# Kernel tuning notes

Hardware: AMD Instinct MI355X
Metric: run time of the kernel (lower is better)

Reference implementation:

```python
import jax, jax.numpy as jnp
import numpy as np

B, L, SD, PD, H, HD, OH = 2, 256, 64, 32, 4, 16, 32
EXP = 64  # MBConv hidden = pair_dim * expand_ratio(2)
SE = 16   # squeezed channels = int(64 * 0.25)


def _ln(x, g, b, eps=1e-5):
    m = jnp.mean(x, -1, keepdims=True)
    v = jnp.mean((x - m) ** 2, -1, keepdims=True)
    return (x - m) / jnp.sqrt(v + eps) * g + b


def _inorm(x, eps=1e-5):  # InstanceNorm2d (no affine), x: [B,C,H,W]
    m = jnp.mean(x, (2, 3), keepdims=True)
    v = jnp.mean((x - m) ** 2, (2, 3), keepdims=True)
    return (x - m) / jnp.sqrt(v + eps)


def setup_inputs() -> dict:
    key = jax.random.key(0)
    ks = jax.random.split(key, 16)
    s = jnp.float32(0.02)
    return dict(
        seq_repr=jax.random.normal(ks[0], (B, L, SD), jnp.float32),
        pair_repr=jax.random.normal(ks[1], (B, L, L, PD), jnp.float32),
        g_attn=jnp.ones((SD,), jnp.float32), b_attn=jnp.zeros((SD,), jnp.float32),
        g_pair=jnp.ones((PD,), jnp.float32), b_pair=jnp.zeros((PD,), jnp.float32),
        W_opm_lin=jax.random.normal(ks[2], (SD, OH), jnp.float32) * s,
        b_opm_lin=jnp.zeros((OH,), jnp.float32),
        g_opm=jnp.ones((OH * OH,), jnp.float32), b_opm=jnp.zeros((OH * OH,), jnp.float32),
        W_opm_proj=jax.random.normal(ks[3], (OH * OH, PD), jnp.float32) * s,
        b_opm_proj=jnp.zeros((PD,), jnp.float32),
        W_exp=jax.random.normal(ks[4], (EXP, PD), jnp.float32) * s,
        W_dw=jax.random.normal(ks[5], (EXP, 1, 3, 3), jnp.float32) * s,
        W_se1=jax.random.normal(ks[6], (SE, EXP), jnp.float32) * s,
        b_se1=jnp.zeros((SE,), jnp.float32),
        W_se2=jax.random.normal(ks[7], (EXP, SE), jnp.float32) * s,
        b_se2=jnp.zeros((EXP,), jnp.float32),
        W_pw=jax.random.normal(ks[8], (PD, EXP), jnp.float32) * s,
        W_qkv=jax.random.normal(ks[9], (SD, 3 * SD), jnp.float32) * s,
        W_outp=jax.random.normal(ks[10], (SD, SD), jnp.float32) * s,
        b_outp=jnp.zeros((SD,), jnp.float32),
        W_bias=jax.random.normal(ks[11], (PD, H), jnp.float32) * s,
    )


def reference(seq_repr, pair_repr, g_attn, b_attn, g_pair, b_pair,
              W_opm_lin, b_opm_lin, g_opm, b_opm, W_opm_proj, b_opm_proj,
              W_exp, W_dw, W_se1, b_se1, W_se2, b_se2, W_pw,
              W_qkv, W_outp, b_outp, W_bias):
    # --- OuterProductMean on attn_norm(seq) ---
    x = _ln(seq_repr, g_attn, b_attn)                            # [B,L,SD]
    a = x @ W_opm_lin + b_opm_lin                                # [B,L,OH]
    outer = jnp.einsum('bid,bje->bijde', a, a).reshape(B, L, L, OH * OH)
    op = _ln(outer, g_opm, b_opm) @ W_opm_proj + b_opm_proj      # [B,L,L,PD]
    pair = pair_repr + op
    # --- MBConv pair processor on pair_norm(pair) ---
    pn = _ln(pair, g_pair, b_pair)
    z0 = jnp.transpose(pn, (0, 3, 1, 2))                         # NCHW [B,PD,L,L]
    h = jax.nn.silu(_inorm(jnp.einsum('bcij,oc->boij', z0, W_exp)))
    h = jax.lax.conv_general_dilated(h, W_dw, (1, 1), 'SAME',
                                     feature_group_count=EXP,
                                     dimension_numbers=('NCHW', 'OIHW', 'NCHW'))
    h = jax.nn.silu(_inorm(h))
    sq = jnp.mean(h, (2, 3), keepdims=True)                      # squeeze [B,EXP,1,1]
    sq = jax.nn.silu(jnp.einsum('bcij,oc->boij', sq, W_se1) + b_se1[None, :, None, None])
    sq = jax.nn.sigmoid(jnp.einsum('bcij,oc->boij', sq, W_se2) + b_se2[None, :, None, None])
    h = h * sq
    h = _inorm(jnp.einsum('bcij,oc->boij', h, W_pw))             # project back to PD
    pair = pair + jnp.transpose(z0 + h, (0, 2, 3, 1))            # MBConv residual + outer residual
    # --- Pairwise-bias attention ---
    pn2 = _ln(pair, g_pair, b_pair)
    bias = jnp.einsum('bijp,ph->bhij', pn2, W_bias)              # [B,H,L,L]
    q, k, v = jnp.split(x @ W_qkv, 3, axis=-1)
    q = q.reshape(B, L, H, HD).transpose(0, 2, 1, 3)
    k = k.reshape(B, L, H, HD).transpose(0, 2, 1, 3)
    v = v.reshape(B, L, H, HD).transpose(0, 2, 1, 3)
    scores = jnp.einsum('bhid,bhjd->bhij', q, k) / jnp.sqrt(jnp.float32(HD)) + bias
    w = jax.nn.softmax(scores, axis=-1)
    ctx = jnp.einsum('bhij,bhjd->bhid', w, v).transpose(0, 2, 1, 3).reshape(B, L, SD)
    seq = seq_repr + ctx @ W_outp + b_outp
    return seq, pair
```

## Files before the change

### kernel.cpp

```cpp
#include <hip/hip_runtime.h>
#include <hip/hip_bf16.h>

#define LLSZ 65536
#define INV_LL (1.f / 65536.f)


__device__ __forceinline__ void chan_stats(const float* sum, const float* sumsq,
                                           int chan, float& m, float& isd)
{
    m = sum[chan] * INV_LL;
    float var = sumsq[chan] * INV_LL - m * m;
    isd = rsqrtf(var + 1e-5f);
}

__device__ __forceinline__ float silu(float t) { return t / (1.f + expf(-t)); }

__global__ __launch_bounds__(256) void kA(
    const float* __restrict__ g_opm, const float* __restrict__ b_opm,
    const float* __restrict__ Wproj, const float* __restrict__ b_proj,
    float* __restrict__ G, float* __restrict__ GW, float* __restrict__ BW,
    float* __restrict__ stats0,
    const float* __restrict__ seq, const float* __restrict__ g_attn,
    const float* __restrict__ b_attn, const float* __restrict__ W_lin,
    const float* __restrict__ b_lin, const float* __restrict__ W_qkv,
    float* __restrict__ a, float* __restrict__ am, float* __restrict__ s2,
    float* __restrict__ qkv)
{
    int tid = threadIdx.x;
    if (blockIdx.x == 0) {
        for (int k = tid; k < 768; k += 256) stats0[k] = 0.f;
        int p = tid & 31, rg = tid >> 5;
        float gw = 0.f, bw = 0.f;
        #pragma unroll 8
        for (int k = 0; k < 128; ++k) {
            int de = k * 8 + rg;
            float wv = Wproj[de * 32 + p];
            float gv = g_opm[de] * wv;
            G[de * 32 + p] = gv;
            gw += gv;
            bw += b_opm[de] * wv;
        }
        __shared__ float rG[256], rB[256];
        rG[rg * 32 + p] = gw;
        rB[rg * 32 + p] = bw;
        __syncthreads();
        for (int s = 4; s > 0; s >>= 1) {
            if (rg < s) {
                rG[rg * 32 + p] += rG[(rg + s) * 32 + p];
                rB[rg * 32 + p] += rB[(rg + s) * 32 + p];
            }
            __syncthreads();
        }
        if (tid < 32) { GW[p] = rG[p]; BW[p] = rB[p] + b_proj[p]; }
    } else {
        __shared__ float Wq[64 * 192];
        __shared__ float Wl[64 * 32];
        __shared__ float xL[4][64];
        #pragma unroll
        for (int k = 0; k < 48; ++k) Wq[k * 256 + tid] = W_qkv[k * 256 + tid];
        #pragma unroll
        for (int k = 0; k < 8; ++k) Wl[k * 256 + tid] = W_lin[k * 256 + tid];
        int sub = tid >> 6, t = tid & 63;
        int row = (blockIdx.x - 1) * 4 + sub;
        float v = seq[row * 64 + t];
        float m = v;
        for (int k = 32; k > 0; k >>= 1) m += __shfl_xor(m, k, 64);
        m *= (1.f / 64.f);
        float d = v - m;
        float var = d * d;
        for (int k = 32; k > 0; k >>= 1) var += __shfl_xor(var, k, 64);
        var *= (1.f / 64.f);
        float x = d * rsqrtf(var + 1e-5f) * g_attn[t] + b_attn[t];
        xL[sub][t] = x;
        __syncthreads();
        if (t < 32) {
            float s = 0.f;
            #pragma unroll
            for (int dd = 0; dd < 64; ++dd) s += xL[sub][dd] * Wl[dd * 32 + t];
            s += b_lin[t];
            a[row * 32 + t] = s;
            float mm = s, ss = s * s;
            for (int k = 16; k > 0; k >>= 1) {
                mm += __shfl_xor(mm, k, 32);
                ss += __shfl_xor(ss, k, 32);
            }
            if (t == 0) { am[row] = mm * (1.f / 32.f); s2[row] = ss * (1.f / 32.f); }
        }
        #pragma unroll
        for (int c3 = 0; c3 < 3; ++c3) {
            int c = c3 * 64 + t;
            float s = 0.f;
            #pragma unroll
            for (int dd = 0; dd < 64; ++dd) s += xL[sub][dd] * Wq[dd * 192 + c];
            qkv[row * 192 + c] = s;
        }
    }
}

__global__ __launch_bounds__(256) void k2_T(
    const float* __restrict__ a, const float* __restrict__ G, float* __restrict__ T)
{
    int row = blockIdx.x;
    int tid = threadIdx.x;
    __shared__ float aL[32];
    if (tid < 32) aL[tid] = a[row * 32 + tid];
    __syncthreads();
    for (int k = 0; k < 4; ++k) {
        int idx = k * 256 + tid;
        float s = 0.f;
        #pragma unroll
        for (int d = 0; d < 32; ++d) s += aL[d] * G[d * 1024 + idx];
        T[row * 1024 + idx] = s;
    }
}

__global__ __launch_bounds__(256) void k3_op(
    const float* __restrict__ a, const float* __restrict__ am,
    const float* __restrict__ s2, const float* __restrict__ T,
    const float* __restrict__ GW, const float* __restrict__ BW,
    const float* __restrict__ pair_in, float* __restrict__ pair1)
{
    int blk = blockIdx.x;
    int row = blk >> 3;
    int jg = blk & 7;
    int b = row >> 8;
    int j0 = jg * 32;
    int tid = threadIdx.x;
    __shared__ float Tl[1024];
    __shared__ float aL[32 * 33];
    __shared__ float amL[32], s2L[32], gwL[32], bwL[32];
    ((float4*)Tl)[tid] = ((const float4*)(T + (long)row * 1024))[tid];
    for (int k = 0; k < 4; ++k) {
        int idx = k * 256 + tid;
        aL[(idx >> 5) * 33 + (idx & 31)] = a[(b * 256 + j0) * 32 + idx];
    }
    if (tid < 32) {
        amL[tid] = am[b * 256 + j0 + tid];
        s2L[tid] = s2[b * 256 + j0 + tid];
        gwL[tid] = GW[tid];
        bwL[tid] = BW[tid];
    }
    __syncthreads();
    int jl = tid >> 3, cq = tid & 7;
    float am_i = am[row], s2_i = s2[row];
    float m = am_i * amL[jl];
    float isd = rsqrtf(s2_i * s2L[jl] - m * m + 1e-5f);
    long base = ((long)row * 256 + j0 + jl) * 32 + cq * 4;
    float4 pv = *(const float4*)(pair_in + base);
    float o[4];
    #pragma unroll
    for (int u = 0; u < 4; ++u) {
        int p = cq * 4 + u;
        float S = 0.f;
        #pragma unroll
        for (int e = 0; e < 32; ++e) S += aL[jl * 33 + e] * Tl[e * 32 + p];
        o[u] = isd * (S - m * gwL[p]) + bwL[p];
    }
    pv.x += o[0]; pv.y += o[1]; pv.z += o[2]; pv.w += o[3];
    *(float4*)(pair1 + base) = pv;
}

__global__ __launch_bounds__(256) void k4_expand(
    const float* __restrict__ pair1, const float* __restrict__ g_pair,
    const float* __restrict__ b_pair, const float* __restrict__ W_exp,
    float* __restrict__ e1, float* __restrict__ st1s, float* __restrict__ st1q)
{
    int blk = blockIdx.x;
    int b = blk >> 10;
    int pixbase = (blk & 1023) * 64;
    int tid = threadIdx.x;
    __shared__ float xL[64 * 33];
    __shared__ float We[2048];
    __shared__ float muL[64], isdL[64];
    __shared__ float gL[32], bL[32];
    for (int k = 0; k < 8; ++k) We[k * 256 + tid] = W_exp[k * 256 + tid];
    if (tid < 32) { gL[tid] = g_pair[tid]; bL[tid] = b_pair[tid]; }
    const float4* src = (const float4*)(pair1 + ((long)b * LLSZ + pixbase) * 32);
    #pragma unroll
    for (int k = 0; k < 2; ++k) {
        int idx = k * 256 + tid;
        float4 v = src[idx];
        int pix = idx >> 3, cq = idx & 7;
        xL[pix * 33 + cq * 4 + 0] = v.x;
        xL[pix * 33 + cq * 4 + 1] = v.y;
        xL[pix * 33 + cq * 4 + 2] = v.z;
        xL[pix * 33 + cq * 4 + 3] = v.w;
    }
    __syncthreads();
    if (tid < 64) {
        float s = 0.f, q = 0.f;
        #pragma unroll
        for (int c = 0; c < 32; ++c) { float v = xL[tid * 33 + c]; s += v; q += v * v; }
        float mu = s * (1.f / 32.f);
        muL[tid] = mu;
        isdL[tid] = rsqrtf(q * (1.f / 32.f) - mu * mu + 1e-5f);
    }
    __syncthreads();
    #pragma unroll
    for (int k = 0; k < 8; ++k) {
        int idx = k * 256 + tid;
        int pix = idx >> 5, c = idx & 31;
        xL[pix * 33 + c] = (xL[pix * 33 + c] - muL[pix]) * isdL[pix] * gL[c] + bL[c];
    }
    __syncthreads();
    int pix = tid & 63, og = tid >> 6;
    float ssk = 0.f, qqk = 0.f;
    for (int oo = 0; oo < 16; ++oo) {
        int o = og * 16 + oo;
        float acc = 0.f;
        #pragma unroll
        for (int c = 0; c < 32; ++c) acc += xL[pix * 33 + c] * We[o * 32 + c];
        e1[((long)(b * 64 + o)) * LLSZ + pixbase + pix] = acc;
        float s = acc, q = acc * acc;
        for (int k = 32; k > 0; k >>= 1) { s += __shfl_xor(s, k, 64); q += __shfl_xor(q, k, 64); }
        if (pix == oo) { ssk = s; qqk = q; }
    }
    if (pix < 16) {
        atomicAdd(&st1s[b * 64 + og * 16 + pix], ssk);
        atomicAdd(&st1q[b * 64 + og * 16 + pix], qqk);
    }
}

__global__ __launch_bounds__(256) void k6_dw(
    const float* __restrict__ e1, const float* __restrict__ st1s,
    const float* __restrict__ st1q, const float* __restrict__ W_dw,
    float* __restrict__ h2, float* __restrict__ st2s, float* __restrict__ st2q)
{
    int blk = blockIdx.x;
    int chan = blk >> 5;
    int r0 = (blk & 31) * 8;
    int o = chan & 63;
    int tid = threadIdx.x;
    float m, isd;
    chan_stats(st1s, st1q, chan, m, isd);
    __shared__ float sL[10][258];
    const float* src = e1 + (long)chan * LLSZ;
    for (int k = tid; k < 640; k += 256) {
        int rr = k >> 6, c4 = k & 63;
        int g = r0 - 1 + rr;
        float4 v = make_float4(0.f, 0.f, 0.f, 0.f);
        bool ok = (g >= 0 && g < 256);
        if (ok) v = *(const float4*)(src + g * 256 + c4 * 4);
        float t;
        t = (v.x - m) * isd; v.x = ok ? silu(t) : 0.f;
        t = (v.y - m) * isd; v.y = ok ? silu(t) : 0.f;
        t = (v.z - m) * isd; v.z = ok ? silu(t) : 0.f;
        t = (v.w - m) * isd; v.w = ok ? silu(t) : 0.f;
        sL[rr][1 + c4 * 4 + 0] = v.x;
        sL[rr][1 + c4 * 4 + 1] = v.y;
        sL[rr][1 + c4 * 4 + 2] = v.z;
        sL[rr][1 + c4 * 4 + 3] = v.w;
    }
    if (tid < 10) { sL[tid][0] = 0.f; sL[tid][257] = 0.f; }
    float w[9];
    #pragma unroll
    for (int k = 0; k < 9; ++k) w[k] = W_dw[o * 9 + k];
    __syncthreads();
    int c = tid;
    float bs = 0.f, bq = 0.f;
    #pragma unroll
    for (int rr = 0; rr < 8; ++rr) {
        float s = 0.f;
        #pragma unroll
        for (int ki = 0; ki < 3; ++ki)
            #pragma unroll
            for (int kj = 0; kj < 3; ++kj)
                s += sL[rr + ki][c + kj] * w[ki * 3 + kj];
        h2[(long)chan * LLSZ + (r0 + rr) * 256 + c] = s;
        bs += s; bq += s * s;
    }
    for (int k = 32; k > 0; k >>= 1) { bs += __shfl_xor(bs, k, 64); bq += __shfl_xor(bq, k, 64); }
    __shared__ float r2s[4], r2q[4];
    int wave = tid >> 6;
    if ((tid & 63) == 0) { r2s[wave] = bs; r2q[wave] = bq; }
    __syncthreads();
    if (tid == 0) {
        atomicAdd(&st2s[chan], r2s[0] + r2s[1] + r2s[2] + r2s[3]);
        atomicAdd(&st2q[chan], r2q[0] + r2q[1] + r2q[2] + r2q[3]);
    }
}

__global__ __launch_bounds__(256) void k8_squeeze(
    const float* __restrict__ h2, const float* __restrict__ st2s,
    const float* __restrict__ st2q, float* __restrict__ sqs)
{
    int bid = blockIdx.x;
    int chan = bid >> 3, seg = bid & 7;
    int tid = threadIdx.x;
    float m, isd;
    chan_stats(st2s, st2q, chan, m, isd);
    const float4* p = (const float4*)(h2 + (long)chan * LLSZ + seg * 8192);
    float s = 0.f;
    #pragma unroll
    for (int k = 0; k < 8; ++k) {
        float4 v = p[k * 256 + tid];
        s += silu((v.x - m) * isd) + silu((v.y - m) * isd)
           + silu((v.z - m) * isd) + silu((v.w - m) * isd);
    }
    for (int k = 32; k > 0; k >>= 1) s += __shfl_xor(s, k, 64);
    __shared__ float rs[4];
    int wave = tid >> 6;
    if ((tid & 63) == 0) rs[wave] = s;
    __syncthreads();
    if (tid == 0) atomicAdd(&sqs[chan], rs[0] + rs[1] + rs[2] + rs[3]);
}

__global__ __launch_bounds__(256) void k10_pw(
    const float* __restrict__ h2, const float* __restrict__ st2s,
    const float* __restrict__ st2q, const float* __restrict__ sqs,
    const float* __restrict__ W_se1, const float* __restrict__ b_se1,
    const float* __restrict__ W_se2, const float* __restrict__ b_se2,
    const float* __restrict__ W_pw, float* __restrict__ hp,
    float* __restrict__ st3s, float* __restrict__ st3q)
{
    int blk = blockIdx.x;
    int b = blk >> 10;
    int pixbase = (blk & 1023) * 64;
    int tid = threadIdx.x;
    __shared__ float hL[64 * 65];
    __shared__ float Wp[2048];
    __shared__ float s1L[16];
    __shared__ float sqvL[64];
    for (int k = 0; k < 8; ++k) Wp[k * 256 + tid] = W_pw[k * 256 + tid];
    if (tid < 16) {
        float s = 0.f;
        for (int c = 0; c < 64; ++c) s += sqs[b * 64 + c] * W_se1[tid * 64 + c];
        s = s * INV_LL + b_se1[tid];
        s1L[tid] = silu(s);
    }
    __syncthreads();
    if (tid < 64) {
        float s = 0.f;
        #pragma unroll
        for (int j = 0; j < 16; ++j) s += s1L[j] * W_se2[tid * 16 + j];
        s += b_se2[tid];
        sqvL[tid] = 1.f / (1.f + expf(-s));
    }
    __syncthreads();
    #pragma unroll
    for (int k = 0; k < 4; ++k) {
        int idx = k * 256 + tid;
        int c = idx >> 4, f4 = idx & 15;
        int chan = b * 64 + c;
        float m, isd;
        chan_stats(st2s, st2q, chan, m, isd);
        float sc = sqvL[c];
        float4 v = *(const float4*)(h2 + (long)chan * LLSZ + pixbase + f4 * 4);
        hL[c * 65 + f4 * 4 + 0] = silu((v.x - m) * isd) * sc;
        hL[c * 65 + f4 * 4 + 1] = silu((v.y - m) * isd) * sc;
        hL[c * 65 + f4 * 4 + 2] = silu((v.z - m) * isd) * sc;
        hL[c * 65 + f4 * 4 + 3] = silu((v.w - m) * isd) * sc;
    }
    __syncthreads();
    int pix = tid & 63, og = tid >> 6;
    float acc[8];
    #pragma unroll
    for (int u = 0; u < 8; ++u) acc[u] = 0.f;
    #pragma unroll
    for (int c = 0; c < 64; ++c) {
        float hv = hL[c * 65 + pix];
        #pragma unroll
        for (int u = 0; u < 8; ++u) acc[u] += hv * Wp[(og * 8 + u) * 64 + c];
    }
    float ssk = 0.f, qqk = 0.f;
    #pragma unroll
    for (int u = 0; u < 8; ++u) {
        float v = acc[u];
        int p = og * 8 + u;
        hp[((long)(b * 32 + p)) * LLSZ + pixbase + pix] = v;
        float s = v, q = v * v;
        for (int k = 32; k > 0; k >>= 1) { s += __shfl_xor(s, k, 64); q += __shfl_xor(q, k, 64); }
        if (pix == u) { ssk = s; qqk = q; }
    }
    if (pix < 8) {
        atomicAdd(&st3s[b * 32 + og * 8 + pix], ssk);
        atomicAdd(&st3q[b * 32 + og * 8 + pix], qqk);
    }
}

__global__ __launch_bounds__(256) void k12_merge(
    const float* __restrict__ pair1, const float* __restrict__ hp,
    const float* __restrict__ st3s, const float* __restrict__ st3q,
    const float* __restrict__ g_pair, const float* __restrict__ b_pair,
    const float* __restrict__ W_bias, float* __restrict__ pair_out,
    float* __restrict__ biasbuf)
{
    int blk = blockIdx.x;
    int b = blk >> 11;
    int pixbase = (blk & 2047) * 32;
    int tid = threadIdx.x;
    __shared__ float hpL[32 * 33];
    {
        int c = tid >> 3, f4 = tid & 7;
        int chan = b * 32 + c;
        float m, isd;
        chan_stats(st3s, st3q, chan, m, isd);
        float4 v = *(const float4*)(hp + (long)chan * LLSZ + pixbase + f4 * 4);
        hpL[c * 33 + f4 * 4 + 0] = (v.x - m) * isd;
        hpL[c * 33 + f4 * 4 + 1] = (v.y - m) * isd;
        hpL[c * 33 + f4 * 4 + 2] = (v.z - m) * isd;
        hpL[c * 33 + f4 * 4 + 3] = (v.w - m) * isd;
    }
    __syncthreads();
    int pg = tid >> 3, cq = tid & 7;
    float gp[4], bp[4], wb[4][4];
    #pragma unroll
    for (int u = 0; u < 4; ++u) {
        int c = cq * 4 + u;
        gp[u] = g_pair[c]; bp[u] = b_pair[c];
        #pragma unroll
        for (int h = 0; h < 4; ++h) wb[u][h] = W_bias[c * 4 + h];
    }
    int pix = pg;
    long base = ((long)b * LLSZ + pixbase + pix) * 32;
    float4 v1 = *(const float4*)(pair1 + base + cq * 4);
    float s = v1.x + v1.y + v1.z + v1.w;
    float q = v1.x * v1.x + v1.y * v1.y + v1.z * v1.z + v1.w * v1.w;
    s += __shfl_xor(s, 1, 8); q += __shfl_xor(q, 1, 8);
    s += __shfl_xor(s, 2, 8); q += __shfl_xor(q, 2, 8);
    s += __shfl_xor(s, 4, 8); q += __shfl_xor(q, 4, 8);
    float mu = s * (1.f / 32.f);
    float isd = rsqrtf(q * (1.f / 32.f) - mu * mu + 1e-5f);
    float vo[4], vv1[4] = {v1.x, v1.y, v1.z, v1.w};
    #pragma unroll
    for (int u = 0; u < 4; ++u) {
        float pnv = (vv1[u] - mu) * isd * gp[u] + bp[u];
        vo[u] = vv1[u] + pnv + hpL[(cq * 4 + u) * 33 + pix];
    }
    *(float4*)(pair_out + base + cq * 4) = make_float4(vo[0], vo[1], vo[2], vo[3]);
    float s2_ = vo[0] + vo[1] + vo[2] + vo[3];
    float q2 = vo[0] * vo[0] + vo[1] * vo[1] + vo[2] * vo[2] + vo[3] * vo[3];
    s2_ += __shfl_xor(s2_, 1, 8); q2 += __shfl_xor(q2, 1, 8);
    s2_ += __shfl_xor(s2_, 2, 8); q2 += __shfl_xor(q2, 2, 8);
    s2_ += __shfl_xor(s2_, 4, 8); q2 += __shfl_xor(q2, 4, 8);
    float mu2 = s2_ * (1.f / 32.f);
    float isd2 = rsqrtf(q2 * (1.f / 32.f) - mu2 * mu2 + 1e-5f);
    float t[4] = {0.f, 0.f, 0.f, 0.f};
    #pragma unroll
    for (int u = 0; u < 4; ++u) {
        float pn2 = (vo[u] - mu2) * isd2 * gp[u] + bp[u];
        #pragma unroll
        for (int h = 0; h < 4; ++h) t[h] += pn2 * wb[u][h];
    }
    #pragma unroll
    for (int h = 0; h < 4; ++h) {
        t[h] += __shfl_xor(t[h], 1, 8);
        t[h] += __shfl_xor(t[h], 2, 8);
        t[h] += __shfl_xor(t[h], 4, 8);
    }
    if (cq == 0) {
        #pragma unroll
        for (int h = 0; h < 4; ++h)
            biasbuf[((long)(b * 4 + h)) * LLSZ + pixbase + pix] = t[h];
    }
}

__global__ __launch_bounds__(256) void k13_attn(
    const float* __restrict__ qkv, const float* __restrict__ biasbuf,
    float* __restrict__ ctx)
{
    int blk = blockIdx.x;
    int b = blk >> 8;
    int h = (blk >> 6) & 3;
    int ig = blk & 63;
    int wave = threadIdx.x >> 6, lane = threadIdx.x & 63;
    int i = ig * 4 + wave;
    const float* qrow = qkv + ((long)(b * 256 + i)) * 192 + h * 16;
    float qv[16];
    #pragma unroll
    for (int d = 0; d < 16; ++d) qv[d] = qrow[d];
    float sj[4];
    #pragma unroll
    for (int q = 0; q < 4; ++q) {
        int j = lane + 64 * q;
        const float* kr = qkv + ((long)(b * 256 + j)) * 192 + 64 + h * 16;
        float s = 0.f;
        #pragma unroll
        for (int d = 0; d < 16; ++d) s += qv[d] * kr[d];
        sj[q] = s * 0.25f + biasbuf[((long)(b * 4 + h)) * LLSZ + i * 256 + j];
    }
    float mx = fmaxf(fmaxf(sj[0], sj[1]), fmaxf(sj[2], sj[3]));
    for (int k = 32; k > 0; k >>= 1) mx = fmaxf(mx, __shfl_xor(mx, k, 64));
    float wgt[4], wsum = 0.f;
    #pragma unroll
    for (int q = 0; q < 4; ++q) { wgt[q] = expf(sj[q] - mx); wsum += wgt[q]; }
    for (int k = 32; k > 0; k >>= 1) wsum += __shfl_xor(wsum, k, 64);
    float inv = 1.f / wsum;
    float o[16];
    #pragma unroll
    for (int d = 0; d < 16; ++d) o[d] = 0.f;
    #pragma unroll
    for (int q = 0; q < 4; ++q) {
        const float* vr = qkv + ((long)(b * 256 + lane + 64 * q)) * 192 + 128 + h * 16;
        #pragma unroll
        for (int d = 0; d < 16; ++d) o[d] += wgt[q] * vr[d];
    }
    #pragma unroll
    for (int d = 0; d < 16; ++d)
        for (int k = 32; k > 0; k >>= 1) o[d] += __shfl_xor(o[d], k, 64);
    if (lane == 0) {
        #pragma unroll
        for (int d = 0; d < 16; ++d)
            ctx[((long)(b * 256 + i)) * 64 + h * 16 + d] = o[d] * inv;
    }
}

__global__ __launch_bounds__(256) void k14_seqout(
    const float* __restrict__ seq, const float* __restrict__ ctx,
    const float* __restrict__ W_outp, const float* __restrict__ b_outp,
    float* __restrict__ out)
{
    __shared__ float Wo[64 * 64];
    __shared__ float cL[4][64];
    int tid = threadIdx.x;
    #pragma unroll
    for (int k = 0; k < 16; ++k) Wo[k * 256 + tid] = W_outp[k * 256 + tid];
    int sub = tid >> 6, t = tid & 63;
    int row = blockIdx.x * 4 + sub;
    cL[sub][t] = ctx[row * 64 + t];
    __syncthreads();
    float s = b_outp[t];
    #pragma unroll
    for (int u = 0; u < 64; ++u) s += cL[sub][u] * Wo[u * 64 + t];
    out[row * 64 + t] = seq[row * 64 + t] + s;
}

extern "C" void kernel_launch(void* const* d_in, const int* in_sizes, int n_in,
                              void* d_out, int out_size, void* d_ws, size_t ws_size,
                              hipStream_t stream) {
    const float* seq_repr   = (const float*)d_in[0];
    const float* pair_repr  = (const float*)d_in[1];
    const float* g_attn     = (const float*)d_in[2];
    const float* b_attn     = (const float*)d_in[3];
    const float* g_pair     = (const float*)d_in[4];
    const float* b_pair     = (const float*)d_in[5];
    const float* W_opm_lin  = (const float*)d_in[6];
    const float* b_opm_lin  = (const float*)d_in[7];
    const float* g_opm      = (const float*)d_in[8];
    const float* b_opm      = (const float*)d_in[9];
    const float* W_opm_proj = (const float*)d_in[10];
    const float* b_opm_proj = (const float*)d_in[11];
    const float* W_exp      = (const float*)d_in[12];
    const float* W_dw       = (const float*)d_in[13];
    const float* W_se1      = (const float*)d_in[14];
    const float* b_se1      = (const float*)d_in[15];
    const float* W_se2      = (const float*)d_in[16];
    const float* b_se2      = (const float*)d_in[17];
    const float* W_pw       = (const float*)d_in[18];
    const float* W_qkv      = (const float*)d_in[19];
    const float* W_outp     = (const float*)d_in[20];
    const float* b_outp     = (const float*)d_in[21];
    const float* W_bias     = (const float*)d_in[22];

    float* out_seq  = (float*)d_out;
    float* out_pair = (float*)d_out + 32768;

    float* w = (float*)d_ws;
    float* a_buf   = w;
    float* am_buf  = a_buf + 16384;
    float* s2_buf  = am_buf + 512;
    float* qkv_buf = s2_buf + 512;
    float* G_buf   = qkv_buf + 98304;
    float* GW_buf  = G_buf + 32768;
    float* BW_buf  = GW_buf + 32;
    float* ctx     = BW_buf + 32;
    float* st1s    = ctx + 32768;
    float* st1q    = st1s + 128;
    float* st2s    = st1q + 128;
    float* st2q    = st2s + 128;
    float* st3s    = st2q + 128;
    float* st3q    = st3s + 64;
    float* sqs     = st3q + 64;
    float* T_buf   = sqs + 128;
    float* biasb   = T_buf;
    float* pair1   = T_buf + 524288;
    float* e1      = pair1 + 4194304;
    float* hp      = e1;
    float* h2      = e1 + 8388608;

    hipLaunchKernelGGL(kA, dim3(129), dim3(256), 0, stream,
                       g_opm, b_opm, W_opm_proj, b_opm_proj, G_buf, GW_buf, BW_buf,
                       st1s,
                       seq_repr, g_attn, b_attn, W_opm_lin, b_opm_lin, W_qkv,
                       a_buf, am_buf, s2_buf, qkv_buf);
    hipLaunchKernelGGL(k2_T, dim3(512), dim3(256), 0, stream, a_buf, G_buf, T_buf);
    hipLaunchKernelGGL(k3_op, dim3(4096), dim3(256), 0, stream,
                       a_buf, am_buf, s2_buf, T_buf, GW_buf, BW_buf,
                       pair_repr, pair1);
    hipLaunchKernelGGL(k4_expand, dim3(2048), dim3(256), 0, stream,
                       pair1, g_pair, b_pair, W_exp, e1, st1s, st1q);
    hipLaunchKernelGGL(k6_dw, dim3(4096), dim3(256), 0, stream,
                       e1, st1s, st1q, W_dw, h2, st2s, st2q);
    hipLaunchKernelGGL(k8_squeeze, dim3(1024), dim3(256), 0, stream,
                       h2, st2s, st2q, sqs);
    hipLaunchKernelGGL(k10_pw, dim3(2048), dim3(256), 0, stream,
                       h2, st2s, st2q, sqs, W_se1, b_se1, W_se2, b_se2,
                       W_pw, hp, st3s, st3q);
    hipLaunchKernelGGL(k12_merge, dim3(4096), dim3(256), 0, stream,
                       pair1, hp, st3s, st3q, g_pair, b_pair, W_bias,
                       out_pair, biasb);
    hipLaunchKernelGGL(k13_attn, dim3(512), dim3(256), 0, stream,
                       qkv_buf, biasb, ctx);
    hipLaunchKernelGGL(k14_seqout, dim3(128), dim3(256), 0, stream,
                       seq_repr, ctx, W_outp, b_outp, out_seq);
}
```

Baseline: 337.2 us.

## Use one pixel per thread for expand, pointwise and merge, with separate stats kernels

The expand, pointwise-projection and merge kernels switch from shared-memory tiles with cross-lane shuffles to a one-pixel-per-thread register layout. Weights are now read straight from global or constant memory instead of being staged in LDS. Instance-norm channel statistics move out of the producing kernels into a separate k_stats reduction pass, launched after both expand and pointwise. This removes shuffles, LDS traffic and per-channel atomics from the main kernels, at the cost of an extra read of e1 and hp, two extra launches, higher register pressure and strided global access for channel-major reads.

```diff
diff --git a/kernel.cpp b/kernel.cpp
--- a/kernel.cpp
+++ b/kernel.cpp
@@ -163,61 +163,61 @@
 __global__ __launch_bounds__(256) void k4_expand(
     const float* __restrict__ pair1, const float* __restrict__ g_pair,
     const float* __restrict__ b_pair, const float* __restrict__ W_exp,
-    float* __restrict__ e1, float* __restrict__ st1s, float* __restrict__ st1q)
-{
-    int blk = blockIdx.x;
-    int b = blk >> 10;
-    int pixbase = (blk & 1023) * 64;
-    int tid = threadIdx.x;
-    __shared__ float xL[64 * 33];
-    __shared__ float We[2048];
-    __shared__ float muL[64], isdL[64];
-    __shared__ float gL[32], bL[32];
-    for (int k = 0; k < 8; ++k) We[k * 256 + tid] = W_exp[k * 256 + tid];
-    if (tid < 32) { gL[tid] = g_pair[tid]; bL[tid] = b_pair[tid]; }
-    const float4* src = (const float4*)(pair1 + ((long)b * LLSZ + pixbase) * 32);
-    #pragma unroll
-    for (int k = 0; k < 2; ++k) {
-        int idx = k * 256 + tid;
-        float4 v = src[idx];
-        int pix = idx >> 3, cq = idx & 7;
-        xL[pix * 33 + cq * 4 + 0] = v.x;
-        xL[pix * 33 + cq * 4 + 1] = v.y;
-        xL[pix * 33 + cq * 4 + 2] = v.z;
-        xL[pix * 33 + cq * 4 + 3] = v.w;
-    }
-    __syncthreads();
-    if (tid < 64) {
-        float s = 0.f, q = 0.f;
-        #pragma unroll
-        for (int c = 0; c < 32; ++c) { float v = xL[tid * 33 + c]; s += v; q += v * v; }
-        float mu = s * (1.f / 32.f);
-        muL[tid] = mu;
-        isdL[tid] = rsqrtf(q * (1.f / 32.f) - mu * mu + 1e-5f);
-    }
-    __syncthreads();
+    float* __restrict__ e1)
+{
+    int b = blockIdx.x >> 9;
+    int oh = (blockIdx.x >> 8) & 1;
+    int px = (blockIdx.x & 255) * 256 + threadIdx.x;
+    long pixel = (long)b * LLSZ + px;
+    float x[32];
+    const float4* src = (const float4*)(pair1 + pixel * 32);
     #pragma unroll
     for (int k = 0; k < 8; ++k) {
-        int idx = k * 256 + tid;
-        int pix = idx >> 5, c = idx & 31;
-        xL[pix * 33 + c] = (xL[pix * 33 + c] - muL[pix]) * isdL[pix] * gL[c] + bL[c];
-    }
-    __syncthreads();
-    int pix = tid & 63, og = tid >> 6;
-    float ssk = 0.f, qqk = 0.f;
-    for (int oo = 0; oo < 16; ++oo) {
-        int o = og * 16 + oo;
+        float4 v = src[k];
+        x[k * 4 + 0] = v.x; x[k * 4 + 1] = v.y;
+        x[k * 4 + 2] = v.z; x[k * 4 + 3] = v.w;
+    }
+    float s = 0.f, q = 0.f;
+    #pragma unroll
+    for (int c = 0; c < 32; ++c) { s += x[c]; q += x[c] * x[c]; }
+    float mu = s * (1.f / 32.f);
+    float isd = rsqrtf(q * (1.f / 32.f) - mu * mu + 1e-5f);
+    #pragma unroll
+    for (int c = 0; c < 32; ++c)
+        x[c] = (x[c] - mu) * isd * g_pair[c] + b_pair[c];
+    float* dst = e1 + ((long)(b * 64 + oh * 32)) * LLSZ + px;
+    #pragma unroll
+    for (int oo = 0; oo < 32; ++oo) {
+        int o = oh * 32 + oo;
         float acc = 0.f;
         #pragma unroll
-        for (int c = 0; c < 32; ++c) acc += xL[pix * 33 + c] * We[o * 32 + c];
-        e1[((long)(b * 64 + o)) * LLSZ + pixbase + pix] = acc;
-        float s = acc, q = acc * acc;
-        for (int k = 32; k > 0; k >>= 1) { s += __shfl_xor(s, k, 64); q += __shfl_xor(q, k, 64); }
-        if (pix == oo) { ssk = s; qqk = q; }
-    }
-    if (pix < 16) {
-        atomicAdd(&st1s[b * 64 + og * 16 + pix], ssk);
-        atomicAdd(&st1q[b * 64 + og * 16 + pix], qqk);
+        for (int c = 0; c < 32; ++c) acc += x[c] * W_exp[o * 32 + c];
+        dst[(long)oo * LLSZ] = acc;
+    }
+}
+
+__global__ __launch_bounds__(256) void k_stats(
+    const float* __restrict__ buf, float* __restrict__ sum, float* __restrict__ sumsq)
+{
+    int bid = blockIdx.x;
+    int chan = bid >> 3, seg = bid & 7;
+    int tid = threadIdx.x;
+    const float4* p = (const float4*)(buf + (long)chan * LLSZ + seg * 8192);
+    float s = 0.f, ss = 0.f;
+    #pragma unroll
+    for (int k = 0; k < 8; ++k) {
+        float4 v = p[k * 256 + tid];
+        s += v.x + v.y + v.z + v.w;
+        ss += v.x * v.x + v.y * v.y + v.z * v.z + v.w * v.w;
+    }
+    for (int k = 32; k > 0; k >>= 1) { s += __shfl_xor(s, k, 64); ss += __shfl_xor(ss, k, 64); }
+    __shared__ float rs[4], rq[4];
+    int wave = tid >> 6;
+    if ((tid & 63) == 0) { rs[wave] = s; rq[wave] = ss; }
+    __syncthreads();
+    if (tid == 0) {
+        atomicAdd(&sum[chan], rs[0] + rs[1] + rs[2] + rs[3]);
+        atomicAdd(&sumsq[chan], rq[0] + rq[1] + rq[2] + rq[3]);
     }
 }
 
@@ -310,18 +310,13 @@
     const float* __restrict__ st2q, const float* __restrict__ sqs,
     const float* __restrict__ W_se1, const float* __restrict__ b_se1,
     const float* __restrict__ W_se2, const float* __restrict__ b_se2,
-    const float* __restrict__ W_pw, float* __restrict__ hp,
-    float* __restrict__ st3s, float* __restrict__ st3q)
-{
-    int blk = blockIdx.x;
-    int b = blk >> 10;
-    int pixbase = (blk & 1023) * 64;
-    int tid = threadIdx.x;
-    __shared__ float hL[64 * 65];
-    __shared__ float Wp[2048];
+    const float* __restrict__ W_pw, float* __restrict__ hp)
+{
+    int b = blockIdx.x >> 8;
+    int px = (blockIdx.x & 255) * 256 + threadIdx.x;
+    int tid = threadIdx.x;
     __shared__ float s1L[16];
     __shared__ float sqvL[64];
-    for (int k = 0; k < 8; ++k) Wp[k * 256 + tid] = W_pw[k * 256 + tid];
     if (tid < 16) {
         float s = 0.f;
         for (int c = 0; c < 64; ++c) s += sqs[b * 64 + c] * W_se1[tid * 64 + c];
@@ -337,44 +332,22 @@
         sqvL[tid] = 1.f / (1.f + expf(-s));
     }
     __syncthreads();
-    #pragma unroll
-    for (int k = 0; k < 4; ++k) {
-        int idx = k * 256 + tid;
-        int c = idx >> 4, f4 = idx & 15;
-        int chan = b * 64 + c;
+    float x[64];
+    const float* src = h2 + ((long)b * 64) * LLSZ + px;
+    #pragma unroll
+    for (int c = 0; c < 64; ++c) {
         float m, isd;
-        chan_stats(st2s, st2q, chan, m, isd);
-        float sc = sqvL[c];
-        float4 v = *(const float4*)(h2 + (long)chan * LLSZ + pixbase + f4 * 4);
-        hL[c * 65 + f4 * 4 + 0] = silu((v.x - m) * isd) * sc;
-        hL[c * 65 + f4 * 4 + 1] = silu((v.y - m) * isd) * sc;
-        hL[c * 65 + f4 * 4 + 2] = silu((v.z - m) * isd) * sc;
-        hL[c * 65 + f4 * 4 + 3] = silu((v.w - m) * isd) * sc;
-    }
-    __syncthreads();
-    int pix = tid & 63, og = tid >> 6;
-    float acc[8];
-    #pragma unroll
-    for (int u = 0; u < 8; ++u) acc[u] = 0.f;
-    #pragma unroll
-    for (int c = 0; c < 64; ++c) {
-        float hv = hL[c * 65 + pix];
-        #pragma unroll
-        for (int u = 0; u < 8; ++u) acc[u] += hv * Wp[(og * 8 + u) * 64 + c];
-    }
-    float ssk = 0.f, qqk = 0.f;
-    #pragma unroll
-    for (int u = 0; u < 8; ++u) {
-        float v = acc[u];
-        int p = og * 8 + u;
-        hp[((long)(b * 32 + p)) * LLSZ + pixbase + pix] = v;
-        float s = v, q = v * v;
-        for (int k = 32; k > 0; k >>= 1) { s += __shfl_xor(s, k, 64); q += __shfl_xor(q, k, 64); }
-        if (pix == u) { ssk = s; qqk = q; }
-    }
-    if (pix < 8) {
-        atomicAdd(&st3s[b * 32 + og * 8 + pix], ssk);
-        atomicAdd(&st3q[b * 32 + og * 8 + pix], qqk);
+        chan_stats(st2s, st2q, b * 64 + c, m, isd);
+        float v = src[(long)c * LLSZ];
+        x[c] = silu((v - m) * isd) * sqvL[c];
+    }
+    float* dst = hp + ((long)b * 32) * LLSZ + px;
+    #pragma unroll
+    for (int p = 0; p < 32; ++p) {
+        float acc = 0.f;
+        #pragma unroll
+        for (int c = 0; c < 64; ++c) acc += x[c] * W_pw[p * 64 + c];
+        dst[(long)p * LLSZ] = acc;
     }
 }
 
@@ -385,74 +358,51 @@
     const float* __restrict__ W_bias, float* __restrict__ pair_out,
     float* __restrict__ biasbuf)
 {
-    int blk = blockIdx.x;
-    int b = blk >> 11;
-    int pixbase = (blk & 2047) * 32;
-    int tid = threadIdx.x;
-    __shared__ float hpL[32 * 33];
-    {
-        int c = tid >> 3, f4 = tid & 7;
-        int chan = b * 32 + c;
-        float m, isd;
-        chan_stats(st3s, st3q, chan, m, isd);
-        float4 v = *(const float4*)(hp + (long)chan * LLSZ + pixbase + f4 * 4);
-        hpL[c * 33 + f4 * 4 + 0] = (v.x - m) * isd;
-        hpL[c * 33 + f4 * 4 + 1] = (v.y - m) * isd;
-        hpL[c * 33 + f4 * 4 + 2] = (v.z - m) * isd;
-        hpL[c * 33 + f4 * 4 + 3] = (v.w - m) * isd;
-    }
-    __syncthreads();
-    int pg = tid >> 3, cq = tid & 7;
-    float gp[4], bp[4], wb[4][4];
-    #pragma unroll
-    for (int u = 0; u < 4; ++u) {
-        int c = cq * 4 + u;
-        gp[u] = g_pair[c]; bp[u] = b_pair[c];
-        #pragma unroll
-        for (int h = 0; h < 4; ++h) wb[u][h] = W_bias[c * 4 + h];
-    }
-    int pix = pg;
-    long base = ((long)b * LLSZ + pixbase + pix) * 32;
-    float4 v1 = *(const float4*)(pair1 + base + cq * 4);
-    float s = v1.x + v1.y + v1.z + v1.w;
-    float q = v1.x * v1.x + v1.y * v1.y + v1.z * v1.z + v1.w * v1.w;
-    s += __shfl_xor(s, 1, 8); q += __shfl_xor(q, 1, 8);
-    s += __shfl_xor(s, 2, 8); q += __shfl_xor(q, 2, 8);
-    s += __shfl_xor(s, 4, 8); q += __shfl_xor(q, 4, 8);
+    int b = blockIdx.x >> 8;
+    int px = (blockIdx.x & 255) * 256 + threadIdx.x;
+    long pixel = (long)b * LLSZ + px;
+    float v1[32];
+    const float4* src = (const float4*)(pair1 + pixel * 32);
+    #pragma unroll
+    for (int k = 0; k < 8; ++k) {
+        float4 v = src[k];
+        v1[k * 4 + 0] = v.x; v1[k * 4 + 1] = v.y;
+        v1[k * 4 + 2] = v.z; v1[k * 4 + 3] = v.w;
+    }
+    float s = 0.f, q = 0.f;
+    #pragma unroll
+    for (int c = 0; c < 32; ++c) { s += v1[c]; q += v1[c] * v1[c]; }
     float mu = s * (1.f / 32.f);
     float isd = rsqrtf(q * (1.f / 32.f) - mu * mu + 1e-5f);
-    float vo[4], vv1[4] = {v1.x, v1.y, v1.z, v1.w};
-    #pragma unroll
-    for (int u = 0; u < 4; ++u) {
-        float pnv = (vv1[u] - mu) * isd * gp[u] + bp[u];
-        vo[u] = vv1[u] + pnv + hpL[(cq * 4 + u) * 33 + pix];
-    }
-    *(float4*)(pair_out + base + cq * 4) = make_float4(vo[0], vo[1], vo[2], vo[3]);
-    float s2_ = vo[0] + vo[1] + vo[2] + vo[3];
-    float q2 = vo[0] * vo[0] + vo[1] * vo[1] + vo[2] * vo[2] + vo[3] * vo[3];
-    s2_ += __shfl_xor(s2_, 1, 8); q2 += __shfl_xor(q2, 1, 8);
-    s2_ += __shfl_xor(s2_, 2, 8); q2 += __shfl_xor(q2, 2, 8);
-    s2_ += __shfl_xor(s2_, 4, 8); q2 += __shfl_xor(q2, 4, 8);
+    float vo[32];
+    const float* hpb = hp + ((long)b * 32) * LLSZ + px;
+    #pragma unroll
+    for (int p = 0; p < 32; ++p) {
+        float m3, isd3;
+        chan_stats(st3s, st3q, b * 32 + p, m3, isd3);
+        float hv = hpb[(long)p * LLSZ];
+        float pnv = (v1[p] - mu) * isd * g_pair[p] + b_pair[p];
+        vo[p] = v1[p] + pnv + (hv - m3) * isd3;
+    }
+    float4* dst = (float4*)(pair_out + pixel * 32);
+    #pragma unroll
+    for (int k = 0; k < 8; ++k)
+        dst[k] = make_float4(vo[k * 4], vo[k * 4 + 1], vo[k * 4 + 2], vo[k * 4 + 3]);
+    float s2_ = 0.f, q2 = 0.f;
+    #pragma unroll
+    for (int c = 0; c < 32; ++c) { s2_ += vo[c]; q2 += vo[c] * vo[c]; }
     float mu2 = s2_ * (1.f / 32.f);
     float isd2 = rsqrtf(q2 * (1.f / 32.f) - mu2 * mu2 + 1e-5f);
     float t[4] = {0.f, 0.f, 0.f, 0.f};
     #pragma unroll
-    for (int u = 0; u < 4; ++u) {
-        float pn2 = (vo[u] - mu2) * isd2 * gp[u] + bp[u];
-        #pragma unroll
-        for (int h = 0; h < 4; ++h) t[h] += pn2 * wb[u][h];
-    }
-    #pragma unroll
-    for (int h = 0; h < 4; ++h) {
-        t[h] += __shfl_xor(t[h], 1, 8);
-        t[h] += __shfl_xor(t[h], 2, 8);
-        t[h] += __shfl_xor(t[h], 4, 8);
-    }
-    if (cq == 0) {
-        #pragma unroll
-        for (int h = 0; h < 4; ++h)
-            biasbuf[((long)(b * 4 + h)) * LLSZ + pixbase + pix] = t[h];
-    }
+    for (int p = 0; p < 32; ++p) {
+        float pn2 = (vo[p] - mu2) * isd2 * g_pair[p] + b_pair[p];
+        #pragma unroll
+        for (int h = 0; h < 4; ++h) t[h] += pn2 * W_bias[p * 4 + h];
+    }
+    #pragma unroll
+    for (int h = 0; h < 4; ++h)
+        biasbuf[((long)(b * 4 + h)) * LLSZ + px] = t[h];
 }
 
 __global__ __launch_bounds__(256) void k13_attn(
@@ -587,16 +537,18 @@
     hipLaunchKernelGGL(k3_op, dim3(4096), dim3(256), 0, stream,
                        a_buf, am_buf, s2_buf, T_buf, GW_buf, BW_buf,
                        pair_repr, pair1);
-    hipLaunchKernelGGL(k4_expand, dim3(2048), dim3(256), 0, stream,
-                       pair1, g_pair, b_pair, W_exp, e1, st1s, st1q);
+    hipLaunchKernelGGL(k4_expand, dim3(1024), dim3(256), 0, stream,
+                       pair1, g_pair, b_pair, W_exp, e1);
+    hipLaunchKernelGGL(k_stats, dim3(1024), dim3(256), 0, stream, e1, st1s, st1q);
     hipLaunchKernelGGL(k6_dw, dim3(4096), dim3(256), 0, stream,
                        e1, st1s, st1q, W_dw, h2, st2s, st2q);
     hipLaunchKernelGGL(k8_squeeze, dim3(1024), dim3(256), 0, stream,
                        h2, st2s, st2q, sqs);
-    hipLaunchKernelGGL(k10_pw, dim3(2048), dim3(256), 0, stream,
+    hipLaunchKernelGGL(k10_pw, dim3(512), dim3(256), 0, stream,
                        h2, st2s, st2q, sqs, W_se1, b_se1, W_se2, b_se2,
-                       W_pw, hp, st3s, st3q);
-    hipLaunchKernelGGL(k12_merge, dim3(4096), dim3(256), 0, stream,
+                       W_pw, hp);
+    hipLaunchKernelGGL(k_stats, dim3(512), dim3(256), 0, stream, hp, st3s, st3q);
+    hipLaunchKernelGGL(k12_merge, dim3(512), dim3(256), 0, stream,
                        pair1, hp, st3s, st3q, g_pair, b_pair, W_bias,
                        out_pair, biasb);
     hipLaunchKernelGGL(k13_attn, dim3(512), dim3(256), 0, stream,
```

Result: faster. 299.8 us (-11.1%).
